# Kernel tuning notes

Hardware: AMD Instinct MI355X
Metric: run time of the kernel (lower is better)

## Reference

```python
import jax, jax.numpy as jnp
import numpy as np

B, N, D_IN, D_MODEL = 8, 384, 512, 512


def gen_masking_matrix(n):
    # Vectorized port of the numba _gen_matrix: a[i, j, k] True iff k lies in the
    # 'geometric attention' reachability band between query i and key j.
    I = np.arange(n)[:, None, None]
    J = np.arange(n)[None, :, None]
    K = np.arange(n)[None, None, :]
    lt = (I < J) & (((K > I) & (K < J)) | ((K >= 2 * I - J + 1) & (K < I)))
    gt = (I > J) & (((K > J) & (K < I)) | ((K > I) & (K <= 2 * I - J)))
    return jnp.asarray(lt | gt)  # (n, n, n) bool


def setup_inputs() -> dict:
    key = jax.random.key(0)
    ks = jax.random.split(key, 8)
    s_in = 1.0 / np.sqrt(D_IN)
    return {
        "h": jax.random.normal(ks[0], (B, N, D_IN), jnp.float32),
        "mask": jnp.ones((B, N), jnp.float32),
        "Wq": jax.random.normal(ks[1], (D_MODEL, D_IN), jnp.float32) * s_in,
        "bq": jax.random.normal(ks[2], (D_MODEL,), jnp.float32) * 0.01,
        "Wk": jax.random.normal(ks[3], (D_MODEL, D_IN), jnp.float32) * s_in,
        "wlr": jax.random.normal(ks[4], (1, D_IN), jnp.float32) * s_in,
        "blr": jnp.zeros((1,), jnp.float32),
        "wrl": jax.random.normal(ks[5], (1, D_IN), jnp.float32) * s_in,
        "brl": jnp.zeros((1,), jnp.float32),
        "alpha": jnp.array([1.0 / np.sqrt(D_MODEL)], jnp.float32),
        "beta": jnp.array([1.0], jnp.float32),
        "gamma": jnp.array([0.0], jnp.float32),
        "masking_matrix": gen_masking_matrix(N),
    }


def reference(h, mask, Wq, bq, Wk, wlr, blr, wrl, brl, alpha, beta, gamma, masking_matrix):
    n = h.shape[1]
    dt = h.dtype
    q = h @ Wq.T + bq                       # (B, n, d_model)
    k = h @ Wk.T                            # (B, n, d_model)
    left = h @ wlr.T + blr                  # (B, n, 1)
    right = h @ wrl.T + brl                 # (B, n, 1)
    iu = jnp.triu(jnp.ones((n, n), dt))
    il = jnp.tril(jnp.ones((n, n), dt), -1)
    d = left * iu + right * il              # (B, n, n)
    scores = jnp.einsum("bnd,bmd->bnm", q, k)
    raw = jnp.clip(alpha * scores + beta * d + gamma, -16.0, 14.0)
    log_p = jax.nn.log_sigmoid(raw)         # log sigmoid(raw)
    log_1mp = jnp.log1p(-jnp.exp(log_p))    # log(1 - sigmoid(raw))
    # a[b,i,j] = sum_k mask[i,j,k] * log_1mp[b,i,k] + log_p[b,i,j]
    a = jnp.einsum("ijk,bik->bij", masking_matrix.astype(dt), log_1mp) + log_p
    r = a - 10000.0 * jnp.eye(n, dtype=dt)
    alignment_mask = mask[:, None, :] * mask[:, :, None]
    return r, alignment_mask
```

## Files before the change

### kernel.cpp

```cpp
#include <hip/hip_runtime.h>
#include <math.h>

#define N_SEQ 384
#define DIM 512
#define BATCH 8
#define M_ROWS (BATCH * N_SEQ)
#define QK_COLS (2 * DIM)

typedef short v8s __attribute__((ext_vector_type(8)));
typedef float v4f __attribute__((ext_vector_type(4)));

__device__ inline unsigned short f2bf(float f) {
    union { float f; unsigned u; } c; c.f = f;
    unsigned u = c.u;
    u += 0x7fffu + ((u >> 16) & 1u);
    return (unsigned short)(u >> 16);
}

#define H_F4   ((M_ROWS * DIM) / 4)
#define W_F4   ((DIM * DIM) / 4)
__global__ __launch_bounds__(256) void cast_inputs(
    const float* __restrict__ h, const float* __restrict__ Wq,
    const float* __restrict__ Wk, unsigned short* __restrict__ h_bf,
    unsigned short* __restrict__ w_bf)
{
    const int idx = blockIdx.x * 256 + threadIdx.x;
    const float4* src; unsigned short* dst; int off;
    if (idx < H_F4)            { src = (const float4*)h;  dst = h_bf;            off = idx; }
    else if (idx < H_F4 + W_F4){ src = (const float4*)Wq; dst = w_bf;            off = idx - H_F4; }
    else                       { src = (const float4*)Wk; dst = w_bf + DIM * DIM/ sizeof(short) * 2; off = idx - H_F4 - W_F4; }
    if (idx >= H_F4 + W_F4) dst = w_bf + (size_t)DIM * DIM;
    float4 v = src[off];
    ushort4 o;
    o.x = f2bf(v.x); o.y = f2bf(v.y); o.z = f2bf(v.z); o.w = f2bf(v.w);
    *(ushort4*)(dst + (size_t)off * 4) = o;
}

__global__ __launch_bounds__(256) void qk_gemm(
    const unsigned short* __restrict__ A,
    const unsigned short* __restrict__ Bm,
    const float* __restrict__ bq,
    unsigned short* __restrict__ C)
{
    __shared__ unsigned short As[128][40];
    __shared__ unsigned short Bs[128][40];
    const int bm = blockIdx.x * 128;
    const int bn = blockIdx.y * 128;
    const int t = threadIdx.x;
    const int wv = t >> 6, lane = t & 63;
    const int wm = (wv & 1) * 64, wn = (wv >> 1) * 64;
    const int lm = lane & 15, quad = lane >> 4;
    const int srow = t >> 2, skc = (t & 3) * 8;
    v4f acc[4][4] = {};
    for (int k0 = 0; k0 < DIM; k0 += 32) {
        v8s a0 = *(const v8s*)(A  + (size_t)(bm + srow)      * DIM + k0 + skc);
        v8s a1 = *(const v8s*)(A  + (size_t)(bm + srow + 64) * DIM + k0 + skc);
        v8s b0 = *(const v8s*)(Bm + (size_t)(bn + srow)      * DIM + k0 + skc);
        v8s b1 = *(const v8s*)(Bm + (size_t)(bn + srow + 64) * DIM + k0 + skc);
        __syncthreads();
        *(v8s*)&As[srow][skc]      = a0;
        *(v8s*)&As[srow + 64][skc] = a1;
        *(v8s*)&Bs[srow][skc]      = b0;
        *(v8s*)&Bs[srow + 64][skc] = b1;
        __syncthreads();
        v8s af[4], bf[4];
#pragma unroll
        for (int i = 0; i < 4; ++i) af[i] = *(const v8s*)&As[wm + i * 16 + lm][quad * 8];
#pragma unroll
        for (int j = 0; j < 4; ++j) bf[j] = *(const v8s*)&Bs[wn + j * 16 + lm][quad * 8];
#pragma unroll
        for (int i = 0; i < 4; ++i)
#pragma unroll
            for (int j = 0; j < 4; ++j)
                acc[i][j] = __builtin_amdgcn_mfma_f32_16x16x32_bf16(af[i], bf[j], acc[i][j], 0, 0, 0);
    }
#pragma unroll
    for (int i = 0; i < 4; ++i)
#pragma unroll
        for (int j = 0; j < 4; ++j) {
            const int col = bn + wn + j * 16 + lm;
            const float bias = (col < DIM) ? bq[col] : 0.f;
#pragma unroll
            for (int r = 0; r < 4; ++r) {
                const int row = bm + wm + i * 16 + quad * 4 + r;
                C[(size_t)row * QK_COLS + col] = f2bf(acc[i][j][r] + bias);
            }
        }
}

__global__ __launch_bounds__(256) void lr_gemv(
    const float* __restrict__ h, const float* __restrict__ wlr,
    const float* __restrict__ blr, const float* __restrict__ wrl,
    const float* __restrict__ brl, float* __restrict__ left,
    float* __restrict__ right)
{
    const int row  = blockIdx.x * 4 + (threadIdx.x >> 6);
    const int lane = threadIdx.x & 63;
    const float* hr = h + (size_t)row * DIM;
    float sl = 0.f, sr = 0.f;
    for (int c = lane; c < DIM; c += 64) {
        const float hv = hr[c];
        sl = fmaf(hv, wlr[c], sl);
        sr = fmaf(hv, wrl[c], sr);
    }
#pragma unroll
    for (int off = 32; off > 0; off >>= 1) {
        sl += __shfl_down(sl, off);
        sr += __shfl_down(sr, off);
    }
    if (lane == 0) {
        left[row]  = sl + blr[0];
        right[row] = sr + brl[0];
    }
}

__global__ __launch_bounds__(256) void score_gemm(
    const unsigned short* __restrict__ QK, const float* __restrict__ left,
    const float* __restrict__ right, const float* __restrict__ alpha,
    const float* __restrict__ beta, const float* __restrict__ gamma,
    float* __restrict__ raw)
{
    __shared__ unsigned short As[64][40];
    __shared__ unsigned short Bs[64][40];
    const int b  = blockIdx.z;
    const int bi = blockIdx.x * 64, bj = blockIdx.y * 64;
    const int t = threadIdx.x;
    const int wv = t >> 6, lane = t & 63;
    const int wm = (wv & 1) * 32, wn = (wv >> 1) * 32;
    const int lm = lane & 15, quad = lane >> 4;
    const int srow = t >> 2, skc = (t & 3) * 8;
    const unsigned short* qb = QK + (size_t)(b * N_SEQ) * QK_COLS;
    v4f acc[2][2] = {};
    for (int k0 = 0; k0 < DIM; k0 += 32) {
        v8s a0 = *(const v8s*)(qb + (size_t)(bi + srow) * QK_COLS + k0 + skc);
        v8s b0 = *(const v8s*)(qb + (size_t)(bj + srow) * QK_COLS + DIM + k0 + skc);
        __syncthreads();
        *(v8s*)&As[srow][skc] = a0;
        *(v8s*)&Bs[srow][skc] = b0;
        __syncthreads();
        v8s af[2], bf[2];
#pragma unroll
        for (int i = 0; i < 2; ++i) af[i] = *(const v8s*)&As[wm + i * 16 + lm][quad * 8];
#pragma unroll
        for (int j = 0; j < 2; ++j) bf[j] = *(const v8s*)&Bs[wn + j * 16 + lm][quad * 8];
#pragma unroll
        for (int i = 0; i < 2; ++i)
#pragma unroll
            for (int j = 0; j < 2; ++j)
                acc[i][j] = __builtin_amdgcn_mfma_f32_16x16x32_bf16(af[i], bf[j], acc[i][j], 0, 0, 0);
    }
    const float al = alpha[0], be = beta[0], ga = gamma[0];
#pragma unroll
    for (int i = 0; i < 2; ++i)
#pragma unroll
        for (int j = 0; j < 2; ++j) {
            const int jcol = bj + wn + j * 16 + lm;
#pragma unroll
            for (int r = 0; r < 4; ++r) {
                const int irow = bi + wm + i * 16 + quad * 4 + r;
                const float lv = left[b * N_SEQ + irow];
                const float rv = right[b * N_SEQ + irow];
                const float dterm = (jcol >= irow) ? lv : rv;
                float v = fmaf(al, acc[i][j][r], fmaf(be, dterm, ga));
                v = fminf(fmaxf(v, -16.f), 14.f);
                raw[((size_t)b * N_SEQ + irow) * N_SEQ + jcol] = v;
            }
        }
}

__global__ __launch_bounds__(384) void finalize(
    const float* __restrict__ raw, const float* __restrict__ mask,
    float* __restrict__ out_r, float* __restrict__ out_am)
{
    const int n = N_SEQ;
    const int i = blockIdx.x;
    const int b = blockIdx.y;
    const int j = threadIdx.x;
    __shared__ float P[N_SEQ + 1];
    __shared__ float wsum[6];
    const float x  = raw[((size_t)b * n + i) * n + j];
    const float lp = -log1pf(expf(-x));
    const float l1 = -log1pf(expf(x));
    const int lane = j & 63, w = j >> 6;
    float v = l1;
#pragma unroll
    for (int off = 1; off < 64; off <<= 1) {
        const float tt = __shfl_up(v, off);
        if (lane >= off) v += tt;
    }
    if (lane == 63) wsum[w] = v;
    __syncthreads();
    float woff = 0.f;
    for (int t = 0; t < w; ++t) woff += wsum[t];
    P[j + 1] = v + woff;
    if (j == 0) P[0] = 0.f;
    __syncthreads();
    float s = 0.f;
    if (i < j) {
        int lo2 = 2 * i - j + 1; if (lo2 < 0) lo2 = 0;
        s = (P[j] - P[i + 1]) + (P[i] - P[lo2]);
    } else if (i > j) {
        int hi2 = 2 * i - j + 1; if (hi2 > n) hi2 = n;
        s = (P[i] - P[j + 1]) + (P[hi2] - P[i + 1]);
    }
    float r = s + lp;
    if (i == j) r -= 10000.f;
    const size_t o = ((size_t)b * n + i) * n + j;
    out_r[o]  = r;
    out_am[o] = mask[b * n + i] * mask[b * n + j];
}

extern "C" void kernel_launch(void* const* d_in, const int* in_sizes, int n_in,
                              void* d_out, int out_size, void* d_ws, size_t ws_size,
                              hipStream_t stream) {
    const float* h     = (const float*)d_in[0];
    const float* mask  = (const float*)d_in[1];
    const float* Wq    = (const float*)d_in[2];
    const float* bq    = (const float*)d_in[3];
    const float* Wk    = (const float*)d_in[4];
    const float* wlr   = (const float*)d_in[5];
    const float* blr   = (const float*)d_in[6];
    const float* wrl   = (const float*)d_in[7];
    const float* brl   = (const float*)d_in[8];
    const float* alpha = (const float*)d_in[9];
    const float* beta  = (const float*)d_in[10];
    const float* gamma = (const float*)d_in[11];

    unsigned short* h_bf  = (unsigned short*)d_ws;
    unsigned short* w_bf  = h_bf + (size_t)M_ROWS * DIM;
    unsigned short* qk_bf = w_bf + (size_t)QK_COLS * DIM;
    float* left  = (float*)(qk_bf + (size_t)M_ROWS * QK_COLS);
    float* right = left + M_ROWS;
    float* raw   = right + M_ROWS;

    float* out_r  = (float*)d_out;
    float* out_am = out_r + (size_t)BATCH * N_SEQ * N_SEQ;

    cast_inputs<<<(H_F4 + 2 * W_F4) / 256, 256, 0, stream>>>(h, Wq, Wk, h_bf, w_bf);
    lr_gemv<<<M_ROWS / 4, 256, 0, stream>>>(h, wlr, blr, wrl, brl, left, right);
    dim3 g1(M_ROWS / 128, QK_COLS / 128);
    qk_gemm<<<g1, 256, 0, stream>>>(h_bf, w_bf, bq, qk_bf);
    dim3 g2(N_SEQ / 64, N_SEQ / 64, BATCH);
    score_gemm<<<g2, 256, 0, stream>>>(qk_bf, left, right, alpha, beta, gamma, raw);
    dim3 g3(N_SEQ, BATCH);
    finalize<<<g3, 384, 0, stream>>>(raw, mask, out_r, out_am);
}
```

Before: 316.8 us.

## Fuse bf16 cast with left/right GEMV, shrink QK GEMM tiles, simplify log-sigmoid

Merges the bf16 cast kernel and the left/right GEMV into a single prep kernel where each wave converts one row and, for h rows, also computes both dot products from the values already loaded. This removes a launch and a second read of h. The QK projection GEMM tile shrinks from 128x128 to 64x64, giving more blocks for the 3072x1024 output at the cost of less reuse per block. In finalize, log_p is derived as x + log(1-sigmoid(x)), saving one exp/log1p pair per element.

```diff
diff --git a/kernel.cpp b/kernel.cpp
--- a/kernel.cpp
+++ b/kernel.cpp
@@ -17,23 +17,52 @@
     return (unsigned short)(u >> 16);
 }
 
-#define H_F4   ((M_ROWS * DIM) / 4)
-#define W_F4   ((DIM * DIM) / 4)
-__global__ __launch_bounds__(256) void cast_inputs(
+__global__ __launch_bounds__(256) void prep(
     const float* __restrict__ h, const float* __restrict__ Wq,
-    const float* __restrict__ Wk, unsigned short* __restrict__ h_bf,
-    unsigned short* __restrict__ w_bf)
-{
-    const int idx = blockIdx.x * 256 + threadIdx.x;
-    const float4* src; unsigned short* dst; int off;
-    if (idx < H_F4)            { src = (const float4*)h;  dst = h_bf;            off = idx; }
-    else if (idx < H_F4 + W_F4){ src = (const float4*)Wq; dst = w_bf;            off = idx - H_F4; }
-    else                       { src = (const float4*)Wk; dst = w_bf + DIM * DIM/ sizeof(short) * 2; off = idx - H_F4 - W_F4; }
-    if (idx >= H_F4 + W_F4) dst = w_bf + (size_t)DIM * DIM;
-    float4 v = src[off];
-    ushort4 o;
-    o.x = f2bf(v.x); o.y = f2bf(v.y); o.z = f2bf(v.z); o.w = f2bf(v.w);
-    *(ushort4*)(dst + (size_t)off * 4) = o;
+    const float* __restrict__ Wk, const float* __restrict__ wlr,
+    const float* __restrict__ blr, const float* __restrict__ wrl,
+    const float* __restrict__ brl, unsigned short* __restrict__ h_bf,
+    unsigned short* __restrict__ w_bf, float* __restrict__ left,
+    float* __restrict__ right)
+{
+    const int wv = threadIdx.x >> 6, lane = threadIdx.x & 63;
+    const int task = blockIdx.x * 4 + wv;
+    const float* src; unsigned short* dst;
+    if (task < M_ROWS) {
+        src = h + (size_t)task * DIM;
+        dst = h_bf + (size_t)task * DIM;
+    } else {
+        const int r = task - M_ROWS;
+        src = (r < DIM) ? (Wq + (size_t)r * DIM) : (Wk + (size_t)(r - DIM) * DIM);
+        dst = w_bf + (size_t)r * DIM;
+    }
+    const float4* s4 = (const float4*)src;
+    const float4 v0 = s4[lane];
+    const float4 v1 = s4[lane + 64];
+    ushort4 o0, o1;
+    o0.x = f2bf(v0.x); o0.y = f2bf(v0.y); o0.z = f2bf(v0.z); o0.w = f2bf(v0.w);
+    o1.x = f2bf(v1.x); o1.y = f2bf(v1.y); o1.z = f2bf(v1.z); o1.w = f2bf(v1.w);
+    *(ushort4*)(dst + lane * 4)       = o0;
+    *(ushort4*)(dst + 256 + lane * 4) = o1;
+    if (task < M_ROWS) {
+        const float4* wl4 = (const float4*)wlr;
+        const float4* wr4 = (const float4*)wrl;
+        const float4 a0 = wl4[lane], a1 = wl4[lane + 64];
+        const float4 c0 = wr4[lane], c1 = wr4[lane + 64];
+        float sl = v0.x * a0.x + v0.y * a0.y + v0.z * a0.z + v0.w * a0.w
+                 + v1.x * a1.x + v1.y * a1.y + v1.z * a1.z + v1.w * a1.w;
+        float sr = v0.x * c0.x + v0.y * c0.y + v0.z * c0.z + v0.w * c0.w
+                 + v1.x * c1.x + v1.y * c1.y + v1.z * c1.z + v1.w * c1.w;
+#pragma unroll
+        for (int off = 32; off > 0; off >>= 1) {
+            sl += __shfl_down(sl, off);
+            sr += __shfl_down(sr, off);
+        }
+        if (lane == 0) {
+            left[task]  = sl + blr[0];
+            right[task] = sr + brl[0];
+        }
+    }
 }
 
 __global__ __launch_bounds__(256) void qk_gemm(
@@ -42,42 +71,38 @@
     const float* __restrict__ bq,
     unsigned short* __restrict__ C)
 {
-    __shared__ unsigned short As[128][40];
-    __shared__ unsigned short Bs[128][40];
-    const int bm = blockIdx.x * 128;
-    const int bn = blockIdx.y * 128;
+    __shared__ unsigned short As[64][40];
+    __shared__ unsigned short Bs[64][40];
+    const int bm = blockIdx.x * 64;
+    const int bn = blockIdx.y * 64;
     const int t = threadIdx.x;
     const int wv = t >> 6, lane = t & 63;
-    const int wm = (wv & 1) * 64, wn = (wv >> 1) * 64;
+    const int wm = (wv & 1) * 32, wn = (wv >> 1) * 32;
     const int lm = lane & 15, quad = lane >> 4;
     const int srow = t >> 2, skc = (t & 3) * 8;
-    v4f acc[4][4] = {};
+    v4f acc[2][2] = {};
     for (int k0 = 0; k0 < DIM; k0 += 32) {
-        v8s a0 = *(const v8s*)(A  + (size_t)(bm + srow)      * DIM + k0 + skc);
-        v8s a1 = *(const v8s*)(A  + (size_t)(bm + srow + 64) * DIM + k0 + skc);
-        v8s b0 = *(const v8s*)(Bm + (size_t)(bn + srow)      * DIM + k0 + skc);
-        v8s b1 = *(const v8s*)(Bm + (size_t)(bn + srow + 64) * DIM + k0 + skc);
-        __syncthreads();
-        *(v8s*)&As[srow][skc]      = a0;
-        *(v8s*)&As[srow + 64][skc] = a1;
-        *(v8s*)&Bs[srow][skc]      = b0;
-        *(v8s*)&Bs[srow + 64][skc] = b1;
-        __syncthreads();
-        v8s af[4], bf[4];
-#pragma unroll
-        for (int i = 0; i < 4; ++i) af[i] = *(const v8s*)&As[wm + i * 16 + lm][quad * 8];
-#pragma unroll
-        for (int j = 0; j < 4; ++j) bf[j] = *(const v8s*)&Bs[wn + j * 16 + lm][quad * 8];
-#pragma unroll
-        for (int i = 0; i < 4; ++i)
-#pragma unroll
-            for (int j = 0; j < 4; ++j)
+        v8s a0 = *(const v8s*)(A  + (size_t)(bm + srow) * DIM + k0 + skc);
+        v8s b0 = *(const v8s*)(Bm + (size_t)(bn + srow) * DIM + k0 + skc);
+        __syncthreads();
+        *(v8s*)&As[srow][skc] = a0;
+        *(v8s*)&Bs[srow][skc] = b0;
+        __syncthreads();
+        v8s af[2], bf[2];
+#pragma unroll
+        for (int i = 0; i < 2; ++i) af[i] = *(const v8s*)&As[wm + i * 16 + lm][quad * 8];
+#pragma unroll
+        for (int j = 0; j < 2; ++j) bf[j] = *(const v8s*)&Bs[wn + j * 16 + lm][quad * 8];
+#pragma unroll
+        for (int i = 0; i < 2; ++i)
+#pragma unroll
+            for (int j = 0; j < 2; ++j)
                 acc[i][j] = __builtin_amdgcn_mfma_f32_16x16x32_bf16(af[i], bf[j], acc[i][j], 0, 0, 0);
     }
 #pragma unroll
-    for (int i = 0; i < 4; ++i)
-#pragma unroll
-        for (int j = 0; j < 4; ++j) {
+    for (int i = 0; i < 2; ++i)
+#pragma unroll
+        for (int j = 0; j < 2; ++j) {
             const int col = bn + wn + j * 16 + lm;
             const float bias = (col < DIM) ? bq[col] : 0.f;
 #pragma unroll
@@ -86,32 +111,6 @@
                 C[(size_t)row * QK_COLS + col] = f2bf(acc[i][j][r] + bias);
             }
         }
-}
-
-__global__ __launch_bounds__(256) void lr_gemv(
-    const float* __restrict__ h, const float* __restrict__ wlr,
-    const float* __restrict__ blr, const float* __restrict__ wrl,
-    const float* __restrict__ brl, float* __restrict__ left,
-    float* __restrict__ right)
-{
-    const int row  = blockIdx.x * 4 + (threadIdx.x >> 6);
-    const int lane = threadIdx.x & 63;
-    const float* hr = h + (size_t)row * DIM;
-    float sl = 0.f, sr = 0.f;
-    for (int c = lane; c < DIM; c += 64) {
-        const float hv = hr[c];
-        sl = fmaf(hv, wlr[c], sl);
-        sr = fmaf(hv, wrl[c], sr);
-    }
-#pragma unroll
-    for (int off = 32; off > 0; off >>= 1) {
-        sl += __shfl_down(sl, off);
-        sr += __shfl_down(sr, off);
-    }
-    if (lane == 0) {
-        left[row]  = sl + blr[0];
-        right[row] = sr + brl[0];
-    }
 }
 
 __global__ __launch_bounds__(256) void score_gemm(
@@ -179,8 +178,8 @@
     __shared__ float P[N_SEQ + 1];
     __shared__ float wsum[6];
     const float x  = raw[((size_t)b * n + i) * n + j];
-    const float lp = -log1pf(expf(-x));
     const float l1 = -log1pf(expf(x));
+    const float lp = x + l1;
     const int lane = j & 63, w = j >> 6;
     float v = l1;
 #pragma unroll
@@ -236,9 +235,9 @@
     float* out_r  = (float*)d_out;
     float* out_am = out_r + (size_t)BATCH * N_SEQ * N_SEQ;
 
-    cast_inputs<<<(H_F4 + 2 * W_F4) / 256, 256, 0, stream>>>(h, Wq, Wk, h_bf, w_bf);
-    lr_gemv<<<M_ROWS / 4, 256, 0, stream>>>(h, wlr, blr, wrl, brl, left, right);
-    dim3 g1(M_ROWS / 128, QK_COLS / 128);
+    prep<<<1024, 256, 0, stream>>>(h, Wq, Wk, wlr, blr, wrl, brl,
+                                   h_bf, w_bf, left, right);
+    dim3 g1(M_ROWS / 64, QK_COLS / 64);
     qk_gemm<<<g1, 256, 0, stream>>>(h_bf, w_bf, bq, qk_bf);
     dim3 g2(N_SEQ / 64, N_SEQ / 64, BATCH);
     score_gemm<<<g2, 256, 0, stream>>>(qk_bf, left, right, alpha, beta, gamma, raw);
```

Result: faster. 306.4 us (-3.3%).
